# Optimization experiments

Measured on AMD Instinct MI355X. Metric: run time of the kernel, lower is better.

Reference implementation:

```python
import jax, jax.numpy as jnp
import numpy as np


def setup_inputs() -> dict:
    key = jax.random.key(0)
    k1, k2 = jax.random.split(key)
    B, S, H, D = 4, 2048, 12, 64
    v = jax.random.normal(k1, (B, S, H, D), dtype=jnp.float32)
    # learned per-head positional weights, sorted ascending along last dim
    # (mirrors torch.sort(torch.randn(H, S), dim=-1)[0])
    w = jnp.sort(jax.random.normal(k2, (H, S), dtype=jnp.float32), axis=-1)
    return {"v": v, "w": w}


def reference(v, w):
    # PositionalBias._naive
    # v: [B, S, H, D]; w: [H, S_max]
    B, S, H, D = v.shape
    seq_len = S - 2  # v[:, 1:-1] is the non-special-token span
    w_ = w[:, :seq_len]  # [H, seq_len]
    # _construct_bias builds bias[h, l, j] = w[h, |l - j|] (symmetric Toeplitz)
    pos = jnp.arange(seq_len)
    idx = jnp.abs(pos[:, None] - pos[None, :])  # [seq_len, seq_len]
    bias = w_[:, idx]  # [H, seq_len, seq_len]
    # zero-pad one row/col on each side -> [H, S, S]
    bias = jnp.pad(bias, ((0, 0), (1, 1), (1, 1)))
    # z_pb: [1, S, H]
    z_pb = jnp.sum(bias, axis=-1).T[None, :, :]
    # pbv: [B, S, H, D]
    pbv = jnp.einsum('nlhd,hlj->njhd', v, bias)
    return (pbv, z_pb)
```

## Files before the change

### kernel.cpp

```cpp
#include <hip/hip_runtime.h>
#include <hip/hip_bf16.h>


typedef short short8 __attribute__((ext_vector_type(8)));
typedef float floatx4 __attribute__((ext_vector_type(4)));
typedef unsigned uint4_ __attribute__((ext_vector_type(4)));

#define QN 4352

__device__ __attribute__((aligned(16))) short g_vt[4 * 12 * 64 * 2048];
__device__ __attribute__((aligned(16))) short g_wt[12 * QN * 8];

__device__ __forceinline__ unsigned short f2bf(float f) {
  union { __hip_bfloat16 b; unsigned short u; } cv;
  cv.b = __float2bfloat16(f);
  return cv.u;
}

__global__ __launch_bounds__(256) void prep_kernel(const float* __restrict__ v,
                                                   const float* __restrict__ w,
                                                   float* __restrict__ out) {
  __shared__ unsigned tls[64 * 65];
  __shared__ float zls[4096];
  __shared__ float wsum[4];

  const int bx  = blockIdx.x;
  const int tid = threadIdx.x;

  if (bx >= 780) {
    const int idx = bx - 780;
    const int h = idx >> 4;
    const int c = idx & 15;
    const float* wh = w + (size_t)h * 2048;
    short* F = g_wt + (size_t)h * QN * 8;
    const int qs = c * 272;
    for (int q = qs + tid; q < qs + 272; q += 256) {
      unsigned short buf[8] __attribute__((aligned(16)));
      #pragma unroll
      for (int i = 0; i < 8; ++i) {
        int t = 2174 - q - i;
        int a = t < 0 ? -t : t;
        buf[i] = (a <= 2045) ? f2bf(wh[a]) : (unsigned short)0;
      }
      *(short8*)&F[(size_t)q * 8] = *(const short8*)buf;
    }
    return;
  }

  if (bx >= 768) {
    const int h = bx - 768;
    float* wvv = zls;
    float* pfx = zls + 2048;
    const float* wh = w + (size_t)h * 2048;
    float* zout = out + 6291456;
    for (int i = tid; i < 2048; i += 256) wvv[i] = (i < 2046) ? wh[i] : 0.f;
    __syncthreads();
    const int base = tid * 8;
    float run0 = 0.f;
    #pragma unroll
    for (int k = 0; k < 8; ++k) run0 += wvv[base + k];
    float x = run0;
    #pragma unroll
    for (int dd = 1; dd < 64; dd <<= 1) {
      float y = __shfl_up(x, dd);
      if ((tid & 63) >= dd) x += y;
    }
    if ((tid & 63) == 63) wsum[tid >> 6] = x;
    __syncthreads();
    const int wid4 = tid >> 6;
    float woff = 0.f;
    #pragma unroll
    for (int u = 0; u < 3; ++u) { float t = wsum[u]; if (u < wid4) woff += t; }
    float pr = x + woff - run0;
    #pragma unroll
    for (int k = 0; k < 8; ++k) { pr += wvv[base + k]; pfx[base + k] = pr; }
    __syncthreads();
    for (int i = tid; i < 2046; i += 256) {
      float z = pfx[i] + pfx[2045 - i] - wvv[0];
      zout[(size_t)(i + 1) * 12 + h] = z;
    }
    if (tid == 0) { zout[h] = 0.f; zout[(size_t)2047 * 12 + h] = 0.f; }
    return;
  }

  const int chunk = bx & 15;
  const int slice = bx >> 4;
  const int n = slice / 12, h = slice - n * 12;
  const int lane = tid & 63;
  const int wv   = tid >> 6;
  const int lbase = chunk * 128 + wv * 32;

  const float* src = v + (((size_t)n * 2048 + lbase) * 12 + h) * 64 + lane;
  #pragma unroll
  for (int kk = 0; kk < 16; ++kk) {
    float f0 = src[(size_t)(2 * kk)     * 768];
    float f1 = src[(size_t)(2 * kk + 1) * 768];
    int l = lbase + 2 * kk;
    unsigned lo = (l == 0)        ? 0u : (unsigned)f2bf(f0);
    unsigned hi = (l + 1 == 2047) ? 0u : (unsigned)f2bf(f1);
    tls[lane * 65 + wv * 16 + kk] = lo | (hi << 16);
  }
  __syncthreads();

  const int r = tid >> 2;
  const int m = tid & 3;
  unsigned xbuf[16];
  #pragma unroll
  for (int k = 0; k < 16; ++k) xbuf[k] = tls[r * 65 + m * 16 + k];
  unsigned* dstu = (unsigned*)(g_vt + (((size_t)n * 12 + h) * 64 + r) * 2048 +
                               (size_t)chunk * 128) + m * 16;
  #pragma unroll
  for (int k4 = 0; k4 < 4; ++k4) {
    uint4_ val = {xbuf[k4 * 4], xbuf[k4 * 4 + 1], xbuf[k4 * 4 + 2], xbuf[k4 * 4 + 3]};
    *(uint4_*)&dstu[k4 * 4] = val;
  }
}

__global__ __launch_bounds__(256, 4) void gemm_kernel(float* __restrict__ out) {
  __shared__ __attribute__((aligned(16))) short Als[2304 * 8];

  const int bx  = blockIdx.x;
  const int tid = threadIdx.x;

  const int slice = bx % 48;
  const int jt    = bx / 48;
  const int ndt = slice & 3;
  const int h   = slice >> 2;
  const int lane = tid & 63;
  const int wid  = tid >> 6;
  const int lm = lane & 15, quad = lane >> 4;
  const int jb = jt * 128;
  const int d  = wid * 16 + lm;

  const short* vtb = g_vt + (((size_t)ndt * 12 + h) * 64 + d) * 2048;
  auto load_bf = [&](int lb) -> short8 {
    return *(const short8*)&vtb[lb];
  };

  short8 bc0 = load_bf(quad * 8);
  short8 bc1 = load_bf(32 + quad * 8);
  short8 bn0 = load_bf(64 + quad * 8);
  short8 bn1 = load_bf(96 + quad * 8);

  const short* wsrc = g_wt + (size_t)h * QN * 8 + (size_t)(2047 - jb) * 8;
  #pragma unroll
  for (int k = 0; k < 9; ++k) {
    *(short8*)&Als[(size_t)(k * 256 + tid) * 8] =
        *(const short8*)&wsrc[(size_t)(k * 256 + tid) * 8];
  }
  __syncthreads();

  const int abase = 127 + quad * 8 - lm;
  auto load_af = [&](int p) -> short8 {
    return *(const short8*)&Als[(size_t)(p + abase) * 8];
  };

  short8 afr[10];
  #pragma unroll
  for (int i = 0; i < 10; ++i) afr[i] = load_af((i - 7) * 16);

  floatx4 acc[8];
  #pragma unroll
  for (int ma = 0; ma < 8; ++ma) acc[ma] = (floatx4){0.f, 0.f, 0.f, 0.f};

  #pragma unroll 4
  for (int t = 0; t < 32; ++t) {
    const int l0 = t * 64;
    int t2 = t + 2; if (t2 > 31) t2 = 31;
    const int lb = t2 * 64 + quad * 8;
    short8 bm0 = load_bf(lb);
    short8 bm1 = load_bf(lb + 32);
    const int l0n = (t < 31) ? l0 + 64 : l0;
    short8 na0 = load_af(l0n - 16);
    short8 na1 = load_af(l0n);
    short8 na2 = load_af(l0n + 16);
    short8 na3 = load_af(l0n + 32);

    __builtin_amdgcn_s_setprio(1);
    #pragma unroll
    for (int ma = 0; ma < 8; ++ma)
      acc[ma] = __builtin_amdgcn_mfma_f32_16x16x32_bf16(afr[7 - ma], bc0, acc[ma], 0, 0, 0);
    #pragma unroll
    for (int ma = 0; ma < 8; ++ma)
      acc[ma] = __builtin_amdgcn_mfma_f32_16x16x32_bf16(afr[9 - ma], bc1, acc[ma], 0, 0, 0);
    __builtin_amdgcn_s_setprio(0);

    #pragma unroll
    for (int i = 0; i < 6; ++i) afr[i] = afr[i + 4];
    afr[6] = na0; afr[7] = na1; afr[8] = na2; afr[9] = na3;
    bc0 = bn0; bc1 = bn1;
    bn0 = bm0; bn1 = bm1;
  }

  float* obase = out + (size_t)ndt * 1572864 + (size_t)h * 64 + d;
  #pragma unroll
  for (int ma = 0; ma < 8; ++ma) {
    floatx4 cc = acc[ma];
    #pragma unroll
    for (int r = 0; r < 4; ++r) {
      int j = jb + ma * 16 + quad * 4 + r;
      float val = (j == 0 || j == 2047) ? 0.f : cc[r];
      obase[(size_t)j * 768] = val;
    }
  }
}

extern "C" void kernel_launch(void* const* d_in, const int* in_sizes, int n_in,
                              void* d_out, int out_size, void* d_ws, size_t ws_size,
                              hipStream_t stream) {
  const float* v = (const float*)d_in[0];
  const float* w = (const float*)d_in[1];
  float* out = (float*)d_out;
  prep_kernel<<<dim3(972), 256, 0, stream>>>(v, w, out);
  gemm_kernel<<<dim3(768), 256, 0, stream>>>(out);
}
```

Baseline: 109.9 us.

## Hand-schedule GEMM main loop with inline asm loads and explicit waitcnts

```diff
diff --git a/kernel.cpp b/kernel.cpp
--- a/kernel.cpp
+++ b/kernel.cpp
@@ -116,7 +116,7 @@
   }
 }
 
-__global__ __launch_bounds__(256, 4) void gemm_kernel(float* __restrict__ out) {
+__global__ __launch_bounds__(256, 3) void gemm_kernel(float* __restrict__ out) {
   __shared__ __attribute__((aligned(16))) short Als[2304 * 8];
 
   const int bx  = blockIdx.x;
@@ -163,19 +163,12 @@
   #pragma unroll
   for (int ma = 0; ma < 8; ++ma) acc[ma] = (floatx4){0.f, 0.f, 0.f, 0.f};
 
-  #pragma unroll 4
-  for (int t = 0; t < 32; ++t) {
-    const int l0 = t * 64;
-    int t2 = t + 2; if (t2 > 31) t2 = 31;
-    const int lb = t2 * 64 + quad * 8;
-    short8 bm0 = load_bf(lb);
-    short8 bm1 = load_bf(lb + 32);
-    const int l0n = (t < 31) ? l0 + 64 : l0;
-    short8 na0 = load_af(l0n - 16);
-    short8 na1 = load_af(l0n);
-    short8 na2 = load_af(l0n + 16);
-    short8 na3 = load_af(l0n + 32);
-
+  unsigned az = (unsigned)(unsigned long long)(&Als[(size_t)abase * 8]) + 768u;
+  unsigned long long vb = (unsigned long long)(const void*)(vtb + quad * 8) + 256ull;
+
+  short8 na0, na1, na2, na3, bm0, bm1;
+
+  auto cluster = [&]() {
     __builtin_amdgcn_s_setprio(1);
     #pragma unroll
     for (int ma = 0; ma < 8; ++ma)
@@ -184,12 +177,49 @@
     for (int ma = 0; ma < 8; ++ma)
       acc[ma] = __builtin_amdgcn_mfma_f32_16x16x32_bf16(afr[9 - ma], bc1, acc[ma], 0, 0, 0);
     __builtin_amdgcn_s_setprio(0);
-
+  };
+  auto rotA = [&]() {
     #pragma unroll
     for (int i = 0; i < 6; ++i) afr[i] = afr[i + 4];
     afr[6] = na0; afr[7] = na1; afr[8] = na2; afr[9] = na3;
+  };
+
+  #pragma unroll 2
+  for (int t = 0; t < 30; ++t) {
+    asm volatile("ds_read_b128 %0, %1 offset:0"   : "=v"(na0) : "v"(az));
+    asm volatile("ds_read_b128 %0, %1 offset:256" : "=v"(na1) : "v"(az));
+    asm volatile("ds_read_b128 %0, %1 offset:512" : "=v"(na2) : "v"(az));
+    asm volatile("ds_read_b128 %0, %1 offset:768" : "=v"(na3) : "v"(az));
+    asm volatile("global_load_dwordx4 %0, %1, off"           : "=v"(bm0) : "v"(vb));
+    asm volatile("global_load_dwordx4 %0, %1, off offset:64" : "=v"(bm1) : "v"(vb));
+    asm volatile("s_waitcnt vmcnt(4)" ::: "memory");
+    __builtin_amdgcn_sched_barrier(0);
+    cluster();
+    asm volatile("s_waitcnt lgkmcnt(0)" ::: "memory");
+    __builtin_amdgcn_sched_barrier(0);
+    rotA();
     bc0 = bn0; bc1 = bn1;
     bn0 = bm0; bn1 = bm1;
+    az += 1024u;
+    vb += 128ull;
+  }
+  {
+    asm volatile("ds_read_b128 %0, %1 offset:0"   : "=v"(na0) : "v"(az));
+    asm volatile("ds_read_b128 %0, %1 offset:256" : "=v"(na1) : "v"(az));
+    asm volatile("ds_read_b128 %0, %1 offset:512" : "=v"(na2) : "v"(az));
+    asm volatile("ds_read_b128 %0, %1 offset:768" : "=v"(na3) : "v"(az));
+    asm volatile("s_waitcnt vmcnt(2)" ::: "memory");
+    __builtin_amdgcn_sched_barrier(0);
+    cluster();
+    asm volatile("s_waitcnt lgkmcnt(0)" ::: "memory");
+    __builtin_amdgcn_sched_barrier(0);
+    rotA();
+    bc0 = bn0; bc1 = bn1;
+  }
+  {
+    asm volatile("s_waitcnt vmcnt(0)" ::: "memory");
+    __builtin_amdgcn_sched_barrier(0);
+    cluster();
   }
 
   float* obase = out + (size_t)ndt * 1572864 + (size_t)h * 64 + d;
```

Measured after the change: 108.0 us. Within noise of the previous version (-1.8%).

## Hand-schedule GEMM main loop with inline asm loads and explicit waitcnts

Applied to the files above, without the earlier changes.

```diff
diff --git a/kernel.cpp b/kernel.cpp
--- a/kernel.cpp
+++ b/kernel.cpp
@@ -116,7 +116,7 @@
   }
 }
 
-__global__ __launch_bounds__(256, 4) void gemm_kernel(float* __restrict__ out) {
+__global__ __launch_bounds__(256, 3) void gemm_kernel(float* __restrict__ out) {
   __shared__ __attribute__((aligned(16))) short Als[2304 * 8];
 
   const int bx  = blockIdx.x;
@@ -133,14 +133,14 @@
   const int d  = wid * 16 + lm;
 
   const short* vtb = g_vt + (((size_t)ndt * 12 + h) * 64 + d) * 2048;
-  auto load_bf = [&](int lb) -> short8 {
-    return *(const short8*)&vtb[lb];
-  };
-
-  short8 bc0 = load_bf(quad * 8);
-  short8 bc1 = load_bf(32 + quad * 8);
-  short8 bn0 = load_bf(64 + quad * 8);
-  short8 bn1 = load_bf(96 + quad * 8);
+
+  short8 afr[16];
+  short8 Bp0[4], Bp1[4];
+
+  Bp0[0] = *(const short8*)&vtb[quad * 8];
+  Bp1[0] = *(const short8*)&vtb[quad * 8 + 32];
+  Bp0[1] = *(const short8*)&vtb[64 + quad * 8];
+  Bp1[1] = *(const short8*)&vtb[64 + quad * 8 + 32];
 
   const short* wsrc = g_wt + (size_t)h * QN * 8 + (size_t)(2047 - jb) * 8;
   #pragma unroll
@@ -151,46 +151,64 @@
   __syncthreads();
 
   const int abase = 127 + quad * 8 - lm;
-  auto load_af = [&](int p) -> short8 {
-    return *(const short8*)&Als[(size_t)(p + abase) * 8];
-  };
-
-  short8 afr[10];
-  #pragma unroll
-  for (int i = 0; i < 10; ++i) afr[i] = load_af((i - 7) * 16);
+  unsigned az0 = (unsigned)(unsigned long long)(&Als[0]) + (unsigned)(abase * 16) - 1792u;
+  unsigned long long vb0 = (unsigned long long)(const void*)(vtb + quad * 8);
 
   floatx4 acc[8];
   #pragma unroll
   for (int ma = 0; ma < 8; ++ma) acc[ma] = (floatx4){0.f, 0.f, 0.f, 0.f};
 
-  #pragma unroll 4
-  for (int t = 0; t < 32; ++t) {
-    const int l0 = t * 64;
-    int t2 = t + 2; if (t2 > 31) t2 = 31;
-    const int lb = t2 * 64 + quad * 8;
-    short8 bm0 = load_bf(lb);
-    short8 bm1 = load_bf(lb + 32);
-    const int l0n = (t < 31) ? l0 + 64 : l0;
-    short8 na0 = load_af(l0n - 16);
-    short8 na1 = load_af(l0n);
-    short8 na2 = load_af(l0n + 16);
-    short8 na3 = load_af(l0n + 32);
-
-    __builtin_amdgcn_s_setprio(1);
-    #pragma unroll
-    for (int ma = 0; ma < 8; ++ma)
-      acc[ma] = __builtin_amdgcn_mfma_f32_16x16x32_bf16(afr[7 - ma], bc0, acc[ma], 0, 0, 0);
-    #pragma unroll
-    for (int ma = 0; ma < 8; ++ma)
-      acc[ma] = __builtin_amdgcn_mfma_f32_16x16x32_bf16(afr[9 - ma], bc1, acc[ma], 0, 0, 0);
-    __builtin_amdgcn_s_setprio(0);
-
-    #pragma unroll
-    for (int i = 0; i < 6; ++i) afr[i] = afr[i + 4];
-    afr[6] = na0; afr[7] = na1; afr[8] = na2; afr[9] = na3;
-    bc0 = bn0; bc1 = bn1;
-    bn0 = bm0; bn1 = bm1;
-  }
+#define A_PRO(D) \
+  asm volatile("ds_read_b128 %0, %1 offset:%2" : "=v"(afr[D]) : "v"(az0), "n"(256 * (D)));
+  A_PRO(0) A_PRO(1) A_PRO(2) A_PRO(3) A_PRO(4)
+  A_PRO(5) A_PRO(6) A_PRO(7) A_PRO(8) A_PRO(9)
+#undef A_PRO
+
+#define G_ITER(T)                                                                        \
+  {                                                                                      \
+    if ((T) < 30) {                                                                      \
+      asm volatile("global_load_dwordx4 %0, %1, off offset:%2"                           \
+                   : "=v"(Bp0[((T) + 2) & 3])                                            \
+                   : "v"(vb0), "n"((((T) < 30 ? (T) + 2 : 0) * 128)));                   \
+      asm volatile("global_load_dwordx4 %0, %1, off offset:%2"                           \
+                   : "=v"(Bp1[((T) + 2) & 3])                                            \
+                   : "v"(vb0), "n"((((T) < 30 ? (T) + 2 : 0) * 128 + 64)));              \
+    }                                                                                    \
+    if ((T) < 31) {                                                                      \
+      asm volatile("ds_read_b128 %0, %1 offset:%2"                                       \
+                   : "=v"(afr[(4 * (T) + 10) & 15])                                      \
+                   : "v"(az0), "n"(((T) < 31 ? 1024 * (T) + 2560 : 0)));                 \
+      asm volatile("ds_read_b128 %0, %1 offset:%2"                                       \
+                   : "=v"(afr[(4 * (T) + 11) & 15])                                      \
+                   : "v"(az0), "n"(((T) < 31 ? 1024 * (T) + 2816 : 0)));                 \
+      asm volatile("ds_read_b128 %0, %1 offset:%2"                                       \
+                   : "=v"(afr[(4 * (T) + 12) & 15])                                      \
+                   : "v"(az0), "n"(((T) < 31 ? 1024 * (T) + 3072 : 0)));                 \
+      asm volatile("ds_read_b128 %0, %1 offset:%2"                                       \
+                   : "=v"(afr[(4 * (T) + 13) & 15])                                      \
+                   : "v"(az0), "n"(((T) < 31 ? 1024 * (T) + 3328 : 0)));                 \
+    }                                                                                    \
+    if ((T) < 30)       asm volatile("s_waitcnt vmcnt(4) lgkmcnt(4)" ::: "memory");      \
+    else if ((T) == 30) asm volatile("s_waitcnt vmcnt(2) lgkmcnt(4)" ::: "memory");      \
+    else                asm volatile("s_waitcnt vmcnt(0) lgkmcnt(0)" ::: "memory");      \
+    __builtin_amdgcn_sched_barrier(0);                                                   \
+    __builtin_amdgcn_s_setprio(1);                                                       \
+    _Pragma("unroll")                                                                    \
+    for (int ma = 0; ma < 8; ++ma)                         \
+      acc[ma] = __builtin_amdgcn_mfma_f32_16x16x32_bf16(                                 \
+          afr[(4 * (T) + 7 - ma) & 15], Bp0[(T) & 3], acc[ma], 0, 0, 0);                 \
+    _Pragma("unroll")                                                                    \
+    for (int ma = 0; ma < 8; ++ma)                        \
+      acc[ma] = __builtin_amdgcn_mfma_f32_16x16x32_bf16(                                 \
+          afr[(4 * (T) + 9 - ma) & 15], Bp1[(T) & 3], acc[ma], 0, 0, 0);                 \
+    __builtin_amdgcn_s_setprio(0);                                                       \
+  }
+
+  G_ITER(0)  G_ITER(1)  G_ITER(2)  G_ITER(3)  G_ITER(4)  G_ITER(5)  G_ITER(6)  G_ITER(7)
+  G_ITER(8)  G_ITER(9)  G_ITER(10) G_ITER(11) G_ITER(12) G_ITER(13) G_ITER(14) G_ITER(15)
+  G_ITER(16) G_ITER(17) G_ITER(18) G_ITER(19) G_ITER(20) G_ITER(21) G_ITER(22) G_ITER(23)
+  G_ITER(24) G_ITER(25) G_ITER(26) G_ITER(27) G_ITER(28) G_ITER(29) G_ITER(30) G_ITER(31)
+#undef G_ITER
 
   float* obase = out + (size_t)ndt * 1572864 + (size_t)h * 64 + d;
   #pragma unroll
```

Measured after the change: 106.7 us (median of 2 runs). 1.03x faster.
